# Optimization experiments

Hardware: AMD Instinct MI355X
Metric: run time of the kernel (lower is better)

Reference implementation:

```python
import jax, jax.numpy as jnp
import numpy as np

N, M, D = 8192, 8192, 64


def setup_inputs() -> dict:
    key = jax.random.key(0)
    kx, ky = jax.random.split(key)
    X = jax.random.normal(kx, (N, D), dtype=jnp.float32)
    Y = jax.random.normal(ky, (M, D), dtype=jnp.float32)
    return {"X": X, "Y": Y}


def reference(X, Y):
    # Pairwise Euclidean distances via the |x|^2 + |y|^2 - 2<x,y> identity
    # (avoids materializing the [N, M, D] difference tensor).
    x2 = jnp.sum(X * X, axis=1)[:, None]          # [N, 1]
    y2 = jnp.sum(Y * Y, axis=1)[None, :]          # [1, M]
    d2 = x2 + y2 - 2.0 * (X @ Y.T)                # [N, M]
    d = jnp.sqrt(jnp.maximum(d2, 0.0))            # Euclidean distance matrix
    dis_1 = jnp.mean(jnp.min(d, axis=1))          # avg over X of nearest-in-Y
    dis_2 = jnp.mean(jnp.min(d, axis=0))          # avg over Y of nearest-in-X
    return dis_1 + dis_2
```

## Files before the change

### kernel.cpp

```cpp
#include <hip/hip_runtime.h>
#include <math.h>


#define NROWS 8192
#define DDIM  64
#define ITILES 64
#define SLICES 16
#define CHUNKS 4
#define LSTR 72

typedef __bf16 bf16_t;
typedef bf16_t bf16x8 __attribute__((ext_vector_type(8)));
typedef float  f32x4  __attribute__((ext_vector_type(4)));


__global__ void prep_kernel(const float* __restrict__ X,
                            const float* __restrict__ Y,
                            bf16_t* __restrict__ Xbf, bf16_t* __restrict__ Ybf,
                            float* __restrict__ x2, float* __restrict__ y2,
                            float* __restrict__ out) {
  int t = blockIdx.x * blockDim.x + threadIdx.x;
  int half = t >> 15;
  int r = (t >> 2) & (NROWS - 1);
  int part = t & 3;
  const float* src = half ? Y : X;
  bf16_t* dst = half ? Ybf : Xbf;
  float* sq = half ? y2 : x2;

  const float4* p = (const float4*)(src + r * DDIM + part * 16);
  float4 v0 = p[0], v1 = p[1], v2 = p[2], v3 = p[3];
  float s = 0.f;
  s = fmaf(v0.x, v0.x, s); s = fmaf(v0.y, v0.y, s);
  s = fmaf(v0.z, v0.z, s); s = fmaf(v0.w, v0.w, s);
  s = fmaf(v1.x, v1.x, s); s = fmaf(v1.y, v1.y, s);
  s = fmaf(v1.z, v1.z, s); s = fmaf(v1.w, v1.w, s);
  s = fmaf(v2.x, v2.x, s); s = fmaf(v2.y, v2.y, s);
  s = fmaf(v2.z, v2.z, s); s = fmaf(v2.w, v2.w, s);
  s = fmaf(v3.x, v3.x, s); s = fmaf(v3.y, v3.y, s);
  s = fmaf(v3.z, v3.z, s); s = fmaf(v3.w, v3.w, s);

  bf16x8 h0 = {(bf16_t)v0.x, (bf16_t)v0.y, (bf16_t)v0.z, (bf16_t)v0.w,
               (bf16_t)v1.x, (bf16_t)v1.y, (bf16_t)v1.z, (bf16_t)v1.w};
  bf16x8 h1 = {(bf16_t)v2.x, (bf16_t)v2.y, (bf16_t)v2.z, (bf16_t)v2.w,
               (bf16_t)v3.x, (bf16_t)v3.y, (bf16_t)v3.z, (bf16_t)v3.w};
  *(bf16x8*)&dst[r * DDIM + part * 16] = h0;
  *(bf16x8*)&dst[r * DDIM + part * 16 + 8] = h1;

  s += __shfl_xor(s, 1, 64);
  s += __shfl_xor(s, 2, 64);
  if (part == 0) sq[r] = s;
  if (t == 0) out[0] = 0.f;
}

__global__ __launch_bounds__(256, 2)
void mine_kernel(const bf16_t* __restrict__ Xbf, const bf16_t* __restrict__ Ybf,
                 const float* __restrict__ x2g, const float* __restrict__ y2g,
                 float* __restrict__ rslab, float* __restrict__ cslab) {
  __shared__ bf16_t Ys[128 * LSTR];

  const int tid = threadIdx.x;
  const int L = tid & 63;
  const int w = tid >> 6;
  const int lr = L & 15;
  const int q = L >> 4;
  const int rh = w >> 1;
  const int ch = w & 1;
  const int itile = blockIdx.x & (ITILES - 1);
  const int slice = blockIdx.x >> 6;
  const int i0 = itile * 128;
  const int rgb = rh * 64;
  const int cgb = ch * 64;
  const int jbase = slice * (CHUNKS * 128);

  bf16x8 Af[8];
#pragma unroll
  for (int a = 0; a < 4; ++a) {
    int row = i0 + rgb + a * 16 + lr;
#pragma unroll
    for (int h = 0; h < 2; ++h)
      Af[a * 2 + h] = *(const bf16x8*)&Xbf[row * DDIM + h * 32 + q * 8];
  }
  float x2r[16];
#pragma unroll
  for (int a = 0; a < 4; ++a) {
    float4 v = *(const float4*)&x2g[i0 + rgb + a * 16 + q * 4];
    x2r[a * 4 + 0] = v.x; x2r[a * 4 + 1] = v.y;
    x2r[a * 4 + 2] = v.z; x2r[a * 4 + 3] = v.w;
  }
  float rmin[16];
#pragma unroll
  for (int k = 0; k < 16; ++k) rmin[k] = INFINITY;

  for (int cc = 0; cc < CHUNKS; ++cc) {
    const int j0 = jbase + cc * 128;
    __syncthreads();
#pragma unroll
    for (int p = 0; p < 4; ++p) {
      int f = p * 256 + tid;
      int r = f >> 3, c = f & 7;
      *(bf16x8*)&Ys[r * LSTR + c * 8] = *(const bf16x8*)&Ybf[(j0 + r) * DDIM + c * 8];
    }
    __syncthreads();

    float y2c[4];
#pragma unroll
    for (int b = 0; b < 4; ++b) y2c[b] = y2g[j0 + cgb + b * 16 + lr];

    f32x4 acc[4][4];
#pragma unroll
    for (int a = 0; a < 4; ++a)
#pragma unroll
      for (int b = 0; b < 4; ++b) acc[a][b] = (f32x4){0.f, 0.f, 0.f, 0.f};

#pragma unroll
    for (int b = 0; b < 4; ++b) {
      bf16x8 B0 = *(const bf16x8*)&Ys[(cgb + b * 16 + lr) * LSTR + q * 8];
      bf16x8 B1 = *(const bf16x8*)&Ys[(cgb + b * 16 + lr) * LSTR + 32 + q * 8];
#pragma unroll
      for (int a = 0; a < 4; ++a) {
        acc[a][b] = __builtin_amdgcn_mfma_f32_16x16x32_bf16(Af[a * 2 + 0], B0, acc[a][b], 0, 0, 0);
        acc[a][b] = __builtin_amdgcn_mfma_f32_16x16x32_bf16(Af[a * 2 + 1], B1, acc[a][b], 0, 0, 0);
      }
    }

    float cmin[4] = {INFINITY, INFINITY, INFINITY, INFINITY};
#pragma unroll
    for (int a = 0; a < 4; ++a)
#pragma unroll
      for (int p = 0; p < 4; ++p) {
        float x2v = x2r[a * 4 + p];
        float rm = rmin[a * 4 + p];
#pragma unroll
        for (int b = 0; b < 4; ++b) {
          float s = acc[a][b][p];
          rm = fminf(rm, fmaf(-2.f, s, y2c[b]));
          cmin[b] = fminf(cmin[b], fmaf(-2.f, s, x2v));
        }
        rmin[a * 4 + p] = rm;
      }
#pragma unroll
    for (int b = 0; b < 4; ++b) {
      cmin[b] = fminf(cmin[b], __shfl_xor(cmin[b], 16, 64));
      cmin[b] = fminf(cmin[b], __shfl_xor(cmin[b], 32, 64));
    }
    float v = cmin[0];
    if (q == 1) v = cmin[1];
    else if (q == 2) v = cmin[2];
    else if (q == 3) v = cmin[3];
    cslab[(itile * 2 + rh) * NROWS + j0 + cgb + L] = v;
  }

#pragma unroll
  for (int a = 0; a < 4; ++a)
#pragma unroll
    for (int p = 0; p < 4; ++p) {
      float v = rmin[a * 4 + p];
      v = fminf(v, __shfl_xor(v, 1, 64));
      v = fminf(v, __shfl_xor(v, 2, 64));
      v = fminf(v, __shfl_xor(v, 4, 64));
      v = fminf(v, __shfl_xor(v, 8, 64));
      if (lr == 0)
        rslab[slice * (NROWS * 2) + (i0 + rgb + a * 16 + q * 4 + p) * 2 + ch] = v;
    }
}

__global__ void reducec_kernel(const float* __restrict__ cslab,
                               float* __restrict__ cmin16) {
  int t = blockIdx.x * blockDim.x + threadIdx.x;
  int g = t >> 13, j = t & (NROWS - 1);
  float m = INFINITY;
#pragma unroll
  for (int k = 0; k < 8; ++k) m = fminf(m, cslab[(g * 8 + k) * NROWS + j]);
  cmin16[g * NROWS + j] = m;
}

__global__ void finish_kernel(const float* __restrict__ x2,
                              const float* __restrict__ y2,
                              const float* __restrict__ rslab,
                              const float* __restrict__ cmin16,
                              float* __restrict__ out) {
  int t = blockIdx.x * blockDim.x + threadIdx.x;
  float d;
  if (t < NROWS) {
    float m = INFINITY;
#pragma unroll
    for (int g = 0; g < SLICES; ++g) {
      float2 v = *(const float2*)&rslab[g * (NROWS * 2) + t * 2];
      m = fminf(m, fminf(v.x, v.y));
    }
    d = sqrtf(fmaxf(x2[t] + m, 0.f));
  } else {
    int j = t - NROWS;
    float m = INFINITY;
#pragma unroll
    for (int g = 0; g < 16; ++g) m = fminf(m, cmin16[g * NROWS + j]);
    d = sqrtf(fmaxf(y2[j] + m, 0.f));
  }
  float v = d * (1.0f / 8192.0f);
#pragma unroll
  for (int off = 32; off > 0; off >>= 1) v += __shfl_down(v, off, 64);
  __shared__ float partial[2];
  if ((threadIdx.x & 63) == 0) partial[threadIdx.x >> 6] = v;
  __syncthreads();
  if (threadIdx.x == 0) atomicAdd(out, partial[0] + partial[1]);
}

extern "C" void kernel_launch(void* const* d_in, const int* in_sizes, int n_in,
                              void* d_out, int out_size, void* d_ws, size_t ws_size,
                              hipStream_t stream) {
  const float* X = (const float*)d_in[0];
  const float* Y = (const float*)d_in[1];
  float* out = (float*)d_out;

  char* wsb = (char*)d_ws;
  bf16_t* Xbf = (bf16_t*)wsb;
  bf16_t* Ybf = (bf16_t*)(wsb + (size_t)NROWS * DDIM * 2);
  float* x2 = (float*)(wsb + 2 * (size_t)NROWS * DDIM * 2);
  float* y2 = x2 + NROWS;
  float* rslab = y2 + NROWS;
  float* cslab = rslab + SLICES * NROWS * 2;
  float* cmin16 = cslab + 128 * NROWS;

  prep_kernel<<<(2 * NROWS * 4) / 256, 256, 0, stream>>>(X, Y, Xbf, Ybf, x2, y2, out);
  mine_kernel<<<ITILES * SLICES, 256, 0, stream>>>(Xbf, Ybf, x2, y2, rslab, cslab);
  reducec_kernel<<<(16 * NROWS) / 256, 256, 0, stream>>>(cslab, cmin16);
  finish_kernel<<<128, 128, 0, stream>>>(x2, y2, rslab, cmin16, out);
}
```

Before: 91.59 us.

## Double-buffer Y tiles in LDS and fuse column reduction into finish kernel

The mine kernel now keeps two LDS buffers for Y chunks. It prefetches the next chunk into registers while MFMAs run on the current one, which drops one barrier per chunk and overlaps global loads with compute. y2 values for all chunks are hoisted into registers up front. The separate reducec kernel is removed: finish_kernel now reduces the 128 column slabs directly with 256-thread blocks, saving a launch and an intermediate write/read. The cost is more LDS and registers per block, which may affect occupancy at 2 blocks per CU.

```diff
diff --git a/kernel.cpp b/kernel.cpp
--- a/kernel.cpp
+++ b/kernel.cpp
@@ -12,7 +12,6 @@
 typedef __bf16 bf16_t;
 typedef bf16_t bf16x8 __attribute__((ext_vector_type(8)));
 typedef float  f32x4  __attribute__((ext_vector_type(4)));
-
 
 __global__ void prep_kernel(const float* __restrict__ X,
                             const float* __restrict__ Y,
@@ -56,7 +55,7 @@
 void mine_kernel(const bf16_t* __restrict__ Xbf, const bf16_t* __restrict__ Ybf,
                  const float* __restrict__ x2g, const float* __restrict__ y2g,
                  float* __restrict__ rslab, float* __restrict__ cslab) {
-  __shared__ bf16_t Ys[128 * LSTR];
+  __shared__ bf16_t Ys[2][128 * LSTR];
 
   const int tid = threadIdx.x;
   const int L = tid & 63;
@@ -87,24 +86,40 @@
     x2r[a * 4 + 0] = v.x; x2r[a * 4 + 1] = v.y;
     x2r[a * 4 + 2] = v.z; x2r[a * 4 + 3] = v.w;
   }
+  float y2all[CHUNKS][4];
+#pragma unroll
+  for (int cc = 0; cc < CHUNKS; ++cc)
+#pragma unroll
+    for (int b = 0; b < 4; ++b)
+      y2all[cc][b] = y2g[jbase + cc * 128 + cgb + b * 16 + lr];
+
   float rmin[16];
 #pragma unroll
   for (int k = 0; k < 16; ++k) rmin[k] = INFINITY;
 
+  bf16x8 Bst[4];
+#pragma unroll
+  for (int p = 0; p < 4; ++p) {
+    int f = p * 256 + tid;
+    Bst[p] = *(const bf16x8*)&Ybf[(jbase + (f >> 3)) * DDIM + (f & 7) * 8];
+  }
+#pragma unroll
+  for (int p = 0; p < 4; ++p) {
+    int f = p * 256 + tid;
+    *(bf16x8*)&Ys[0][(f >> 3) * LSTR + (f & 7) * 8] = Bst[p];
+  }
+  __syncthreads();
+
   for (int cc = 0; cc < CHUNKS; ++cc) {
-    const int j0 = jbase + cc * 128;
-    __syncthreads();
-#pragma unroll
-    for (int p = 0; p < 4; ++p) {
-      int f = p * 256 + tid;
-      int r = f >> 3, c = f & 7;
-      *(bf16x8*)&Ys[r * LSTR + c * 8] = *(const bf16x8*)&Ybf[(j0 + r) * DDIM + c * 8];
-    }
-    __syncthreads();
-
-    float y2c[4];
-#pragma unroll
-    for (int b = 0; b < 4; ++b) y2c[b] = y2g[j0 + cgb + b * 16 + lr];
+    const bf16_t* Yb = Ys[cc & 1];
+    if (cc + 1 < CHUNKS) {
+      int j0n = jbase + (cc + 1) * 128;
+#pragma unroll
+      for (int p = 0; p < 4; ++p) {
+        int f = p * 256 + tid;
+        Bst[p] = *(const bf16x8*)&Ybf[(j0n + (f >> 3)) * DDIM + (f & 7) * 8];
+      }
+    }
 
     f32x4 acc[4][4];
 #pragma unroll
@@ -114,8 +129,8 @@
 
 #pragma unroll
     for (int b = 0; b < 4; ++b) {
-      bf16x8 B0 = *(const bf16x8*)&Ys[(cgb + b * 16 + lr) * LSTR + q * 8];
-      bf16x8 B1 = *(const bf16x8*)&Ys[(cgb + b * 16 + lr) * LSTR + 32 + q * 8];
+      bf16x8 B0 = *(const bf16x8*)&Yb[(cgb + b * 16 + lr) * LSTR + q * 8];
+      bf16x8 B1 = *(const bf16x8*)&Yb[(cgb + b * 16 + lr) * LSTR + 32 + q * 8];
 #pragma unroll
       for (int a = 0; a < 4; ++a) {
         acc[a][b] = __builtin_amdgcn_mfma_f32_16x16x32_bf16(Af[a * 2 + 0], B0, acc[a][b], 0, 0, 0);
@@ -133,7 +148,7 @@
 #pragma unroll
         for (int b = 0; b < 4; ++b) {
           float s = acc[a][b][p];
-          rm = fminf(rm, fmaf(-2.f, s, y2c[b]));
+          rm = fminf(rm, fmaf(-2.f, s, y2all[cc][b]));
           cmin[b] = fminf(cmin[b], fmaf(-2.f, s, x2v));
         }
         rmin[a * 4 + p] = rm;
@@ -147,7 +162,17 @@
     if (q == 1) v = cmin[1];
     else if (q == 2) v = cmin[2];
     else if (q == 3) v = cmin[3];
-    cslab[(itile * 2 + rh) * NROWS + j0 + cgb + L] = v;
+    cslab[(itile * 2 + rh) * NROWS + jbase + cc * 128 + cgb + L] = v;
+
+    if (cc + 1 < CHUNKS) {
+      bf16_t* Yn = Ys[(cc + 1) & 1];
+#pragma unroll
+      for (int p = 0; p < 4; ++p) {
+        int f = p * 256 + tid;
+        *(bf16x8*)&Yn[(f >> 3) * LSTR + (f & 7) * 8] = Bst[p];
+      }
+      __syncthreads();
+    }
   }
 
 #pragma unroll
@@ -164,45 +189,48 @@
     }
 }
 
-__global__ void reducec_kernel(const float* __restrict__ cslab,
-                               float* __restrict__ cmin16) {
-  int t = blockIdx.x * blockDim.x + threadIdx.x;
-  int g = t >> 13, j = t & (NROWS - 1);
-  float m = INFINITY;
-#pragma unroll
-  for (int k = 0; k < 8; ++k) m = fminf(m, cslab[(g * 8 + k) * NROWS + j]);
-  cmin16[g * NROWS + j] = m;
-}
-
 __global__ void finish_kernel(const float* __restrict__ x2,
                               const float* __restrict__ y2,
                               const float* __restrict__ rslab,
-                              const float* __restrict__ cmin16,
+                              const float* __restrict__ cslab,
                               float* __restrict__ out) {
-  int t = blockIdx.x * blockDim.x + threadIdx.x;
-  float d;
-  if (t < NROWS) {
+  const int b = blockIdx.x;
+  const int tid = threadIdx.x;
+  if (b < 32) {
+    int row = b * 256 + tid;
     float m = INFINITY;
 #pragma unroll
     for (int g = 0; g < SLICES; ++g) {
-      float2 v = *(const float2*)&rslab[g * (NROWS * 2) + t * 2];
+      float2 v = *(const float2*)&rslab[g * (NROWS * 2) + row * 2];
       m = fminf(m, fminf(v.x, v.y));
     }
-    d = sqrtf(fmaxf(x2[t] + m, 0.f));
+    float v = sqrtf(fmaxf(x2[row] + m, 0.f)) * (1.0f / 8192.0f);
+#pragma unroll
+    for (int off = 32; off > 0; off >>= 1) v += __shfl_down(v, off, 64);
+    __shared__ float partial[4];
+    if ((tid & 63) == 0) partial[tid >> 6] = v;
+    __syncthreads();
+    if (tid == 0)
+      atomicAdd(out, partial[0] + partial[1] + partial[2] + partial[3]);
   } else {
-    int j = t - NROWS;
+    int j = (b - 32) * 64 + (tid & 63);
+    int seg = tid >> 6;
     float m = INFINITY;
 #pragma unroll
-    for (int g = 0; g < 16; ++g) m = fminf(m, cmin16[g * NROWS + j]);
-    d = sqrtf(fmaxf(y2[j] + m, 0.f));
-  }
-  float v = d * (1.0f / 8192.0f);
-#pragma unroll
-  for (int off = 32; off > 0; off >>= 1) v += __shfl_down(v, off, 64);
-  __shared__ float partial[2];
-  if ((threadIdx.x & 63) == 0) partial[threadIdx.x >> 6] = v;
-  __syncthreads();
-  if (threadIdx.x == 0) atomicAdd(out, partial[0] + partial[1]);
+    for (int k = 0; k < 32; ++k)
+      m = fminf(m, cslab[(seg * 32 + k) * NROWS + j]);
+    __shared__ float red[4][64];
+    red[seg][tid & 63] = m;
+    __syncthreads();
+    if (tid < 64) {
+      float mc = fminf(fminf(red[0][tid], red[1][tid]),
+                       fminf(red[2][tid], red[3][tid]));
+      float v = sqrtf(fmaxf(y2[j] + mc, 0.f)) * (1.0f / 8192.0f);
+#pragma unroll
+      for (int off = 32; off > 0; off >>= 1) v += __shfl_down(v, off, 64);
+      if (tid == 0) atomicAdd(out, v);
+    }
+  }
 }
 
 extern "C" void kernel_launch(void* const* d_in, const int* in_sizes, int n_in,
@@ -219,10 +247,8 @@
   float* y2 = x2 + NROWS;
   float* rslab = y2 + NROWS;
   float* cslab = rslab + SLICES * NROWS * 2;
-  float* cmin16 = cslab + 128 * NROWS;
 
   prep_kernel<<<(2 * NROWS * 4) / 256, 256, 0, stream>>>(X, Y, Xbf, Ybf, x2, y2, out);
   mine_kernel<<<ITILES * SLICES, 256, 0, stream>>>(Xbf, Ybf, x2, y2, rslab, cslab);
-  reducec_kernel<<<(16 * NROWS) / 256, 256, 0, stream>>>(cslab, cmin16);
-  finish_kernel<<<128, 128, 0, stream>>>(x2, y2, rslab, cmin16, out);
-}
+  finish_kernel<<<160, 256, 0, stream>>>(x2, y2, rslab, cslab, out);
+}
```

Result: faster. 85.03 us (-7.2%).
